# Kernel optimization log

Measured on AMD Instinct MI355X. Metric: run time of the kernel, lower is better.

The kernel has to match this reference:

```python
import jax, jax.numpy as jnp
import numpy as np

N_NODES = 50000
N_EDGES = 800000
IN_DIM = 128
HEADS = 4
OUT_DIM = 32
NEG_SLOPE = 0.2


def setup_inputs() -> dict:
    key = jax.random.key(0)
    k_x, k_e, k_w, k_as, k_ad = jax.random.split(key, 5)
    x = jax.random.normal(k_x, (N_NODES, IN_DIM), dtype=jnp.float32)
    edge_index = jax.random.randint(k_e, (2, N_EDGES), 0, N_NODES, dtype=jnp.int32)
    # Linear(in_dim, heads*out_dim, bias=False): store as [in_dim, heads*out_dim]
    W = jax.random.normal(k_w, (IN_DIM, HEADS * OUT_DIM), dtype=jnp.float32) * 0.05
    a_src = jax.random.normal(k_as, (HEADS, OUT_DIM), dtype=jnp.float32) * 0.01
    a_dst = jax.random.normal(k_ad, (HEADS, OUT_DIM), dtype=jnp.float32) * 0.01
    return {"x": x, "edge_index": edge_index, "W": W, "a_src": a_src, "a_dst": a_dst}


def reference(x, edge_index, W, a_src, a_dst):
    N = x.shape[0]
    H, D = a_src.shape
    src, dst = edge_index[0], edge_index[1]
    h = (x @ W).reshape(N, H, D)                      # [N, H, D]
    h_src = h[src]                                    # [E, H, D] gather
    h_dst = h[dst]                                    # [E, H, D] gather
    e = jnp.einsum('ehd,hd->eh', h_src, a_src) + jnp.einsum('ehd,hd->eh', h_dst, a_dst)
    e = jax.nn.leaky_relu(e, NEG_SLOPE)               # [E, H]
    # segment softmax over dst, per head (vectorized across heads)
    m = jax.ops.segment_max(e, dst, num_segments=N)   # [N, H]
    exp = jnp.exp(e - m[dst])                         # [E, H]
    s = jax.ops.segment_sum(exp, dst, num_segments=N) # [N, H]
    alpha = exp / (s[dst] + 1e-12)                    # [E, H]
    # dropout p=0.0 -> identity
    out = jax.ops.segment_sum(alpha[:, :, None] * h_src, dst, num_segments=N)  # [N, H, D]
    return out.mean(axis=1)                           # [N, D]
```

## Files before the change

### kernel.cpp

```cpp
#include <hip/hip_runtime.h>
#include <hip/hip_bf16.h>

#define IN_DIM 128
#define HEADS 4
#define ODIM 32
#define HD (HEADS * ODIM)
#define NEG_SLOPE 0.2f

#define GM 64
#define LDK 136

#define BIN_SHIFT 5
#define BIN_NODES 32
#define BINCAP 1024
#define MAXBINS 2048
#define KE 16

#define SMEM_BYTES 52224

typedef unsigned short ushortT;
typedef __attribute__((ext_vector_type(8))) short bf16x8;
typedef __attribute__((ext_vector_type(4))) float f32x4;

static __device__ __forceinline__ ushortT f2bf(float f) {
    __hip_bfloat16 b = __float2bfloat16(f);
    return *reinterpret_cast<ushortT*>(&b);
}
static __device__ __forceinline__ float bf2f(ushortT u) {
    unsigned int x = ((unsigned int)u) << 16;
    return __uint_as_float(x);
}
static __device__ __forceinline__ float hsel(float4 v, int head) {
    return (head == 0) ? v.x : (head == 1) ? v.y : (head == 2) ? v.z : v.w;
}

__global__ void __launch_bounds__(256) k_wconv_zero(
    const float* __restrict__ W, ushortT* __restrict__ Wt_g,
    int* __restrict__ bin_cursor, int nbins)
{
    const int idx = blockIdx.x * 256 + threadIdx.x;
    const int c = idx >> 7, k = idx & 127;
    Wt_g[c * 128 + k] = f2bf(W[k * HD + c]);
    if (idx < nbins) bin_cursor[idx] = 0;
}

__global__ void __launch_bounds__(256) k_mega(
    const float* __restrict__ x, const ushortT* __restrict__ Wt_g,
    const float* __restrict__ a_src, const float* __restrict__ a_dst,
    const int* __restrict__ src, const int* __restrict__ dst,
    ushortT* __restrict__ h_bf, float* __restrict__ s_src, float* __restrict__ s_dst,
    int* __restrict__ bin_cursor, int* __restrict__ bin_buf,
    int N, int E, int nbins, int nBinBlocks)
{
    __shared__ __align__(16) char smem[SMEM_BYTES];
    const int t = threadIdx.x;

    if ((int)blockIdx.x < nBinBlocks) {
        int* lcnt = reinterpret_cast<int*>(smem);
        int* lcur = lcnt + MAXBINS;
        for (int i = t; i < nbins; i += 256) lcnt[i] = 0;
        __syncthreads();

        const int base_e = blockIdx.x * (256 * KE);
        int b_[KE]; int p_[KE];
#pragma unroll
        for (int k = 0; k < KE; ++k) {
            const int e = base_e + k * 256 + t;
            if (e < E) {
                const int d = dst[e];
                const int s = src[e];
                b_[k] = d >> BIN_SHIFT;
                p_[k] = ((d & (BIN_NODES - 1)) << 16) | s;
                atomicAdd(&lcnt[b_[k]], 1);
            } else {
                b_[k] = -1;
            }
        }
        __syncthreads();
        for (int i = t; i < nbins; i += 256) {
            const int c = lcnt[i];
            lcur[i] = (c > 0) ? atomicAdd(&bin_cursor[i], c) : 0;
        }
        __syncthreads();
#pragma unroll
        for (int k = 0; k < KE; ++k) {
            if (b_[k] >= 0) {
                const int pos = atomicAdd(&lcur[b_[k]], 1);
                if (pos < BINCAP) bin_buf[b_[k] * BINCAP + pos] = p_[k];
            }
        }
        return;
    }

    ushortT* Xs = reinterpret_cast<ushortT*>(smem);
    ushortT* Wt = Xs + GM * LDK;

    const int n0 = ((int)blockIdx.x - nBinBlocks) * GM;

    {
#pragma unroll
        for (int it = 0; it < 8; ++it) {
            const int o = it * 2048 + t * 8;
            *reinterpret_cast<uint4*>(&Wt[(o >> 7) * LDK + (o & 127)]) =
                *reinterpret_cast<const uint4*>(&Wt_g[o]);
        }
    }
    {
        const int r  = t >> 2;
        const int k0 = (t & 3) * 32;
        const int ng = n0 + r;
        if (ng < N) {
#pragma unroll
            for (int kk = 0; kk < 32; kk += 4) {
                float4 v = *reinterpret_cast<const float4*>(
                    &x[(size_t)ng * IN_DIM + k0 + kk]);
                ushort4 u;
                u.x = f2bf(v.x); u.y = f2bf(v.y); u.z = f2bf(v.z); u.w = f2bf(v.w);
                *reinterpret_cast<ushort4*>(&Xs[r * LDK + k0 + kk]) = u;
            }
        } else {
#pragma unroll
            for (int kk = 0; kk < 32; kk += 4)
                *reinterpret_cast<ushort4*>(&Xs[r * LDK + k0 + kk]) =
                    make_ushort4(0, 0, 0, 0);
        }
    }
    __syncthreads();

    const int w  = t >> 6;
    const int l  = t & 63;
    const int lr = l & 15;
    const int lk = (l >> 4) * 8;

    f32x4 acc[8];
#pragma unroll
    for (int i = 0; i < 8; ++i) acc[i] = (f32x4)(0.f);

#pragma unroll
    for (int kt = 0; kt < 4; ++kt) {
        const bf16x8 af = *reinterpret_cast<const bf16x8*>(
            &Xs[(w * 16 + lr) * LDK + kt * 32 + lk]);
#pragma unroll
        for (int ct = 0; ct < 8; ++ct) {
            const bf16x8 bfr = *reinterpret_cast<const bf16x8*>(
                &Wt[(ct * 16 + lr) * LDK + kt * 32 + lk]);
            acc[ct] = __builtin_amdgcn_mfma_f32_16x16x32_bf16(af, bfr, acc[ct],
                                                              0, 0, 0);
        }
    }

    float aSv[8], aDv[8];
#pragma unroll
    for (int ct = 0; ct < 8; ++ct) {
        aSv[ct] = a_src[ct * 16 + lr];
        aDv[ct] = a_dst[ct * 16 + lr];
    }

    const int rbase = w * 16 + (l >> 4) * 4;

#pragma unroll
    for (int j = 0; j < 4; ++j) {
        const int ng = n0 + rbase + j;

        if (ng < N) {
#pragma unroll
            for (int ct = 0; ct < 8; ++ct)
                h_bf[(size_t)ng * HD + ct * 16 + lr] = f2bf(acc[ct][j]);
        }

        float ps[4] = {0.f, 0.f, 0.f, 0.f}, pd[4] = {0.f, 0.f, 0.f, 0.f};
#pragma unroll
        for (int ct = 0; ct < 8; ++ct) {
            ps[ct >> 1] = fmaf(acc[ct][j], aSv[ct], ps[ct >> 1]);
            pd[ct >> 1] = fmaf(acc[ct][j], aDv[ct], pd[ct >> 1]);
        }
#pragma unroll
        for (int o = 1; o <= 8; o <<= 1) {
#pragma unroll
            for (int hh = 0; hh < 4; ++hh) {
                ps[hh] += __shfl_xor(ps[hh], o, 64);
                pd[hh] += __shfl_xor(pd[hh], o, 64);
            }
        }
        if (lr == 0 && ng < N) {
            *reinterpret_cast<float4*>(&s_src[ng * 4]) =
                make_float4(ps[0], ps[1], ps[2], ps[3]);
            *reinterpret_cast<float4*>(&s_dst[ng * 4]) =
                make_float4(pd[0], pd[1], pd[2], pd[3]);
        }
    }
}

__global__ void __launch_bounds__(256) k_pull_binned(
    const int* __restrict__ bin_buf, const int* __restrict__ bin_cursor,
    const ushortT* __restrict__ h_bf,
    const float* __restrict__ s_src, const float* __restrict__ s_dst,
    float* __restrict__ out, int N)
{
    __shared__ ushortT csr[BINCAP];
    __shared__ int cnt_s[BIN_NODES], start_s[BIN_NODES], cur_s[BIN_NODES];

    const int b = blockIdx.x;
    const int t = threadIdx.x;
    const int node0 = b << BIN_SHIFT;

    int nedge = bin_cursor[b];
    nedge = (nedge < BINCAP) ? nedge : BINCAP;

    if (t < BIN_NODES) cnt_s[t] = 0;
    __syncthreads();

    for (int i = t; i < nedge; i += 256)
        atomicAdd(&cnt_s[bin_buf[b * BINCAP + i] >> 16], 1);
    __syncthreads();

    if (t < 32) {
        const int v = cnt_s[t];
        int inc = v;
#pragma unroll
        for (int o = 1; o < 32; o <<= 1) {
            const int x = __shfl_up(inc, o, 32);
            if (t >= o) inc += x;
        }
        start_s[t] = inc - v;
        cur_s[t]   = inc - v;
    }
    __syncthreads();

    for (int i = t; i < nedge; i += 256) {
        const int p = bin_buf[b * BINCAP + i];
        const int pos = atomicAdd(&cur_s[p >> 16], 1);
        csr[pos] = (ushortT)(p & 0xFFFF);
    }
    __syncthreads();

    const int wv   = t >> 6;
    const int l    = t & 63;
    const int half = l >> 5;
    const int l32  = l & 31;
    const int head = l32 >> 3;
    const int hoff = head * 8 + (l32 & 7);

    const ushort4* h4  = reinterpret_cast<const ushort4*>(h_bf);
    const float4*  ss4 = reinterpret_cast<const float4*>(s_src);

    for (int k = 0; k < 8; ++k) {
        const int nloc = wv * 8 + k;
        const int n = node0 + nloc;
        if (n >= N) break;

        const int st  = start_s[nloc];
        const int deg = cnt_s[nloc];
        const float4 vd4 = reinterpret_cast<const float4*>(s_dst)[n];
        const float vd = hsel(vd4, head);

        float den = 0.f;
        float a0 = 0.f, a1 = 0.f, a2 = 0.f, a3 = 0.f;

        const int count = (deg - half + 1) >> 1;
        for (int j = 0; j < count; j += 4) {
            const int i0 = st + 2 * j + half;
            const bool v1 = (j + 1) < count;
            const bool v2 = (j + 2) < count;
            const bool v3 = (j + 3) < count;
            const int s0 = csr[i0];
            const int s1 = v1 ? csr[i0 + 2] : s0;
            const int s2 = v2 ? csr[i0 + 4] : s0;
            const int s3 = v3 ? csr[i0 + 6] : s0;

            const float4 w0 = ss4[s0];
            const float4 w1 = ss4[s1];
            const float4 w2 = ss4[s2];
            const float4 w3 = ss4[s3];
            const ushort4 q0 = h4[(size_t)s0 * 32 + hoff];
            const ushort4 q1 = h4[(size_t)s1 * 32 + hoff];
            const ushort4 q2 = h4[(size_t)s2 * 32 + hoff];
            const ushort4 q3 = h4[(size_t)s3 * 32 + hoff];

            float e0 = hsel(w0, head) + vd;
            float e1 = hsel(w1, head) + vd;
            float e2 = hsel(w2, head) + vd;
            float e3 = hsel(w3, head) + vd;
            e0 = (e0 > 0.f) ? e0 : NEG_SLOPE * e0;
            e1 = (e1 > 0.f) ? e1 : NEG_SLOPE * e1;
            e2 = (e2 > 0.f) ? e2 : NEG_SLOPE * e2;
            e3 = (e3 > 0.f) ? e3 : NEG_SLOPE * e3;
            const float x0 = __expf(e0);
            const float x1 = v1 ? __expf(e1) : 0.f;
            const float x2 = v2 ? __expf(e2) : 0.f;
            const float x3 = v3 ? __expf(e3) : 0.f;

            den += (x0 + x1) + (x2 + x3);
            a0 = fmaf(x0, bf2f(q0.x), a0); a1 = fmaf(x0, bf2f(q0.y), a1);
            a2 = fmaf(x0, bf2f(q0.z), a2); a3 = fmaf(x0, bf2f(q0.w), a3);
            a0 = fmaf(x1, bf2f(q1.x), a0); a1 = fmaf(x1, bf2f(q1.y), a1);
            a2 = fmaf(x1, bf2f(q1.z), a2); a3 = fmaf(x1, bf2f(q1.w), a3);
            a0 = fmaf(x2, bf2f(q2.x), a0); a1 = fmaf(x2, bf2f(q2.y), a1);
            a2 = fmaf(x2, bf2f(q2.z), a2); a3 = fmaf(x2, bf2f(q2.w), a3);
            a0 = fmaf(x3, bf2f(q3.x), a0); a1 = fmaf(x3, bf2f(q3.y), a1);
            a2 = fmaf(x3, bf2f(q3.z), a2); a3 = fmaf(x3, bf2f(q3.w), a3);
        }

        a0 += __shfl_xor(a0, 32, 64);
        a1 += __shfl_xor(a1, 32, 64);
        a2 += __shfl_xor(a2, 32, 64);
        a3 += __shfl_xor(a3, 32, 64);
        den += __shfl_xor(den, 32, 64);

        const float inv = 1.f / (den + 1e-12f);
        a0 *= inv; a1 *= inv; a2 *= inv; a3 *= inv;

        a0 += __shfl_xor(a0, 8, 64);  a0 += __shfl_xor(a0, 16, 64);
        a1 += __shfl_xor(a1, 8, 64);  a1 += __shfl_xor(a1, 16, 64);
        a2 += __shfl_xor(a2, 8, 64);  a2 += __shfl_xor(a2, 16, 64);
        a3 += __shfl_xor(a3, 8, 64);  a3 += __shfl_xor(a3, 16, 64);

        if (l < 8) {
            float4 o4 = make_float4(0.25f * a0, 0.25f * a1, 0.25f * a2, 0.25f * a3);
            *reinterpret_cast<float4*>(&out[(size_t)n * ODIM + l * 4]) = o4;
        }
    }
}

extern "C" void kernel_launch(void* const* d_in, const int* in_sizes, int n_in,
                              void* d_out, int out_size, void* d_ws, size_t ws_size,
                              hipStream_t stream)
{
    const float* x      = (const float*)d_in[0];
    const int*   eidx   = (const int*)d_in[1];
    const float* W      = (const float*)d_in[2];
    const float* a_src  = (const float*)d_in[3];
    const float* a_dst  = (const float*)d_in[4];
    float* out = (float*)d_out;

    const int N = in_sizes[0] / IN_DIM;
    const int E = in_sizes[1] / 2;
    const int* src = eidx;
    const int* dst = eidx + E;

    const int nbins = (N + BIN_NODES - 1) >> BIN_SHIFT;

    char* wsp = (char*)d_ws;
    ushortT* h_bf   = (ushortT*)wsp;  wsp += (size_t)N * HD * sizeof(ushortT);
    float* s_src    = (float*)wsp;    wsp += (size_t)N * HEADS * sizeof(float);
    float* s_dst    = (float*)wsp;    wsp += (size_t)N * HEADS * sizeof(float);
    ushortT* Wt_g   = (ushortT*)wsp;  wsp += (size_t)128 * 128 * sizeof(ushortT);
    int* bin_buf    = (int*)wsp;      wsp += (size_t)nbins * BINCAP * sizeof(int);
    int* bin_cursor = (int*)wsp;      wsp += (size_t)nbins * sizeof(int);

    k_wconv_zero<<<64, 256, 0, stream>>>(W, Wt_g, bin_cursor, nbins);

    {
        const int epb = 256 * KE;
        const int nBinBlocks  = (E + epb - 1) / epb;
        const int nGemmBlocks = (N + GM - 1) / GM;
        k_mega<<<nBinBlocks + nGemmBlocks, 256, 0, stream>>>(
            x, Wt_g, a_src, a_dst, src, dst,
            h_bf, s_src, s_dst, bin_cursor, bin_buf,
            N, E, nbins, nBinBlocks);
    }

    k_pull_binned<<<nbins, 256, 0, stream>>>(bin_buf, bin_cursor, h_bf,
                                             s_src, s_dst, out, N);
}
```

Before: 79.60 us.

## Quantize projected node features to int8 with per-node scale for gather

The GEMM epilogue now stages the accumulator tile in shared memory, computes a per-node absmax scale, and stores h as int8 with one float scale per node instead of bf16. The pull kernel gathers 4-byte packed int8 words plus a scale per neighbour, and folds the scale into the softmax weight. This halves the bytes moved by the random edge gathers, which dominate the aggregation kernel. In exchange it adds an extra scale load per edge, extra shared-memory staging and syncs in the GEMM, and a drop in precision to int8.

```diff
diff --git a/kernel.cpp b/kernel.cpp
--- a/kernel.cpp
+++ b/kernel.cpp
@@ -9,6 +9,7 @@
 
 #define GM 64
 #define LDK 136
+#define ACCW 132
 
 #define BIN_SHIFT 5
 #define BIN_NODES 32
@@ -26,12 +27,11 @@
     __hip_bfloat16 b = __float2bfloat16(f);
     return *reinterpret_cast<ushortT*>(&b);
 }
-static __device__ __forceinline__ float bf2f(ushortT u) {
-    unsigned int x = ((unsigned int)u) << 16;
-    return __uint_as_float(x);
-}
 static __device__ __forceinline__ float hsel(float4 v, int head) {
     return (head == 0) ? v.x : (head == 1) ? v.y : (head == 2) ? v.z : v.w;
+}
+static __device__ __forceinline__ float i8f(unsigned int p, int sh) {
+    return (float)((int)(p << (24 - sh)) >> 24);
 }
 
 __global__ void __launch_bounds__(256) k_wconv_zero(
@@ -48,7 +48,8 @@
     const float* __restrict__ x, const ushortT* __restrict__ Wt_g,
     const float* __restrict__ a_src, const float* __restrict__ a_dst,
     const int* __restrict__ src, const int* __restrict__ dst,
-    ushortT* __restrict__ h_bf, float* __restrict__ s_src, float* __restrict__ s_dst,
+    unsigned char* __restrict__ h8, float* __restrict__ scales,
+    float* __restrict__ s_src, float* __restrict__ s_dst,
     int* __restrict__ bin_cursor, int* __restrict__ bin_buf,
     int N, int E, int nbins, int nBinBlocks)
 {
@@ -155,19 +156,11 @@
         aSv[ct] = a_src[ct * 16 + lr];
         aDv[ct] = a_dst[ct * 16 + lr];
     }
-
     const int rbase = w * 16 + (l >> 4) * 4;
 
 #pragma unroll
     for (int j = 0; j < 4; ++j) {
         const int ng = n0 + rbase + j;
-
-        if (ng < N) {
-#pragma unroll
-            for (int ct = 0; ct < 8; ++ct)
-                h_bf[(size_t)ng * HD + ct * 16 + lr] = f2bf(acc[ct][j]);
-        }
-
         float ps[4] = {0.f, 0.f, 0.f, 0.f}, pd[4] = {0.f, 0.f, 0.f, 0.f};
 #pragma unroll
         for (int ct = 0; ct < 8; ++ct) {
@@ -189,11 +182,57 @@
                 make_float4(pd[0], pd[1], pd[2], pd[3]);
         }
     }
+
+    __syncthreads();
+    float* accb = reinterpret_cast<float*>(smem);
+
+#pragma unroll
+    for (int ct = 0; ct < 8; ++ct)
+#pragma unroll
+        for (int j = 0; j < 4; ++j)
+            accb[(rbase + j) * ACCW + ct * 16 + lr] = acc[ct][j];
+    __syncthreads();
+
+    {
+        const int row = t >> 2;
+        const int c0  = (t & 3) * 32;
+        const int ng  = n0 + row;
+
+        float4 v[8];
+        float m = 0.f;
+#pragma unroll
+        for (int i = 0; i < 8; ++i) {
+            v[i] = *reinterpret_cast<const float4*>(&accb[row * ACCW + c0 + 4 * i]);
+            m = fmaxf(m, fmaxf(fmaxf(fabsf(v[i].x), fabsf(v[i].y)),
+                               fmaxf(fabsf(v[i].z), fabsf(v[i].w))));
+        }
+        m = fmaxf(m, __shfl_xor(m, 1, 64));
+        m = fmaxf(m, __shfl_xor(m, 2, 64));
+
+        const float inv = (m > 0.f) ? 127.f / m : 0.f;
+        unsigned int p[8];
+#pragma unroll
+        for (int i = 0; i < 8; ++i) {
+            const int q0 = __float2int_rn(v[i].x * inv);
+            const int q1 = __float2int_rn(v[i].y * inv);
+            const int q2 = __float2int_rn(v[i].z * inv);
+            const int q3 = __float2int_rn(v[i].w * inv);
+            p[i] = (q0 & 0xFF) | ((q1 & 0xFF) << 8) |
+                   ((q2 & 0xFF) << 16) | ((q3 & 0xFF) << 24);
+        }
+        if (ng < N) {
+            *reinterpret_cast<uint4*>(&h8[(size_t)ng * 128 + c0]) =
+                make_uint4(p[0], p[1], p[2], p[3]);
+            *reinterpret_cast<uint4*>(&h8[(size_t)ng * 128 + c0 + 16]) =
+                make_uint4(p[4], p[5], p[6], p[7]);
+            if ((t & 3) == 0) scales[ng] = m * (1.f / 127.f);
+        }
+    }
 }
 
 __global__ void __launch_bounds__(256) k_pull_binned(
     const int* __restrict__ bin_buf, const int* __restrict__ bin_cursor,
-    const ushortT* __restrict__ h_bf,
+    const unsigned char* __restrict__ h8, const float* __restrict__ scales,
     const float* __restrict__ s_src, const float* __restrict__ s_dst,
     float* __restrict__ out, int N)
 {
@@ -241,8 +280,8 @@
     const int head = l32 >> 3;
     const int hoff = head * 8 + (l32 & 7);
 
-    const ushort4* h4  = reinterpret_cast<const ushort4*>(h_bf);
-    const float4*  ss4 = reinterpret_cast<const float4*>(s_src);
+    const unsigned int* hu = reinterpret_cast<const unsigned int*>(h8);
+    const float4* ss4 = reinterpret_cast<const float4*>(s_src);
 
     for (int k = 0; k < 8; ++k) {
         const int nloc = wv * 8 + k;
@@ -272,10 +311,14 @@
             const float4 w1 = ss4[s1];
             const float4 w2 = ss4[s2];
             const float4 w3 = ss4[s3];
-            const ushort4 q0 = h4[(size_t)s0 * 32 + hoff];
-            const ushort4 q1 = h4[(size_t)s1 * 32 + hoff];
-            const ushort4 q2 = h4[(size_t)s2 * 32 + hoff];
-            const ushort4 q3 = h4[(size_t)s3 * 32 + hoff];
+            const float sc0 = scales[s0];
+            const float sc1 = scales[s1];
+            const float sc2 = scales[s2];
+            const float sc3 = scales[s3];
+            const unsigned int q0 = hu[(size_t)s0 * 32 + hoff];
+            const unsigned int q1 = hu[(size_t)s1 * 32 + hoff];
+            const unsigned int q2 = hu[(size_t)s2 * 32 + hoff];
+            const unsigned int q3 = hu[(size_t)s3 * 32 + hoff];
 
             float e0 = hsel(w0, head) + vd;
             float e1 = hsel(w1, head) + vd;
@@ -291,14 +334,19 @@
             const float x3 = v3 ? __expf(e3) : 0.f;
 
             den += (x0 + x1) + (x2 + x3);
-            a0 = fmaf(x0, bf2f(q0.x), a0); a1 = fmaf(x0, bf2f(q0.y), a1);
-            a2 = fmaf(x0, bf2f(q0.z), a2); a3 = fmaf(x0, bf2f(q0.w), a3);
-            a0 = fmaf(x1, bf2f(q1.x), a0); a1 = fmaf(x1, bf2f(q1.y), a1);
-            a2 = fmaf(x1, bf2f(q1.z), a2); a3 = fmaf(x1, bf2f(q1.w), a3);
-            a0 = fmaf(x2, bf2f(q2.x), a0); a1 = fmaf(x2, bf2f(q2.y), a1);
-            a2 = fmaf(x2, bf2f(q2.z), a2); a3 = fmaf(x2, bf2f(q2.w), a3);
-            a0 = fmaf(x3, bf2f(q3.x), a0); a1 = fmaf(x3, bf2f(q3.y), a1);
-            a2 = fmaf(x3, bf2f(q3.z), a2); a3 = fmaf(x3, bf2f(q3.w), a3);
+            const float ws0 = x0 * sc0;
+            const float ws1 = x1 * sc1;
+            const float ws2 = x2 * sc2;
+            const float ws3 = x3 * sc3;
+
+            a0 = fmaf(ws0, i8f(q0, 0), a0);  a1 = fmaf(ws0, i8f(q0, 8), a1);
+            a2 = fmaf(ws0, i8f(q0, 16), a2); a3 = fmaf(ws0, i8f(q0, 24), a3);
+            a0 = fmaf(ws1, i8f(q1, 0), a0);  a1 = fmaf(ws1, i8f(q1, 8), a1);
+            a2 = fmaf(ws1, i8f(q1, 16), a2); a3 = fmaf(ws1, i8f(q1, 24), a3);
+            a0 = fmaf(ws2, i8f(q2, 0), a0);  a1 = fmaf(ws2, i8f(q2, 8), a1);
+            a2 = fmaf(ws2, i8f(q2, 16), a2); a3 = fmaf(ws2, i8f(q2, 24), a3);
+            a0 = fmaf(ws3, i8f(q3, 0), a0);  a1 = fmaf(ws3, i8f(q3, 8), a1);
+            a2 = fmaf(ws3, i8f(q3, 16), a2); a3 = fmaf(ws3, i8f(q3, 24), a3);
         }
 
         a0 += __shfl_xor(a0, 32, 64);
@@ -341,7 +389,8 @@
     const int nbins = (N + BIN_NODES - 1) >> BIN_SHIFT;
 
     char* wsp = (char*)d_ws;
-    ushortT* h_bf   = (ushortT*)wsp;  wsp += (size_t)N * HD * sizeof(ushortT);
+    unsigned char* h8 = (unsigned char*)wsp; wsp += (size_t)N * 128;
+    float* scales   = (float*)wsp;    wsp += (size_t)N * sizeof(float);
     float* s_src    = (float*)wsp;    wsp += (size_t)N * HEADS * sizeof(float);
     float* s_dst    = (float*)wsp;    wsp += (size_t)N * HEADS * sizeof(float);
     ushortT* Wt_g   = (ushortT*)wsp;  wsp += (size_t)128 * 128 * sizeof(ushortT);
@@ -356,10 +405,10 @@
         const int nGemmBlocks = (N + GM - 1) / GM;
         k_mega<<<nBinBlocks + nGemmBlocks, 256, 0, stream>>>(
             x, Wt_g, a_src, a_dst, src, dst,
-            h_bf, s_src, s_dst, bin_cursor, bin_buf,
+            h8, scales, s_src, s_dst, bin_cursor, bin_buf,
             N, E, nbins, nBinBlocks);
     }
 
-    k_pull_binned<<<nbins, 256, 0, stream>>>(bin_buf, bin_cursor, h_bf,
+    k_pull_binned<<<nbins, 256, 0, stream>>>(bin_buf, bin_cursor, h8, scales,
                                              s_src, s_dst, out, N);
 }
```

Result: faster. 74.00 us (-7.0%).
